# Kernel tuning notes

Hardware: AMD Instinct MI355X
Metric: run time of the kernel (lower is better)

Reference implementation:

```python
import jax, jax.numpy as jnp
import numpy as np

ALPHA = 0.2  # LeakyReLU negative slope
NEG_BIG = -9e15


def setup_inputs() -> dict:
    key = jax.random.key(0)
    k1, k2, k3, k4 = jax.random.split(key, 4)
    B, N, Fin, Fout = 16, 1024, 256, 256
    h = jax.random.normal(k1, (B, N, Fin), dtype=jnp.float32)
    adj = jax.random.randint(k2, (B, N, N), 0, 2, dtype=jnp.int32)
    # xavier_uniform with gain=1.414
    def xavier(k, shape, gain=1.414):
        fan_in, fan_out = shape[0], shape[1]
        bound = gain * np.sqrt(6.0 / (fan_in + fan_out))
        return jax.random.uniform(k, shape, jnp.float32, -bound, bound)
    W = xavier(k3, (Fin, Fout))
    a = xavier(k4, (2 * Fout, 1))
    return {"h": h, "adj": adj, "W": W, "a": a}


def reference(h, adj, W, a):
    # h: [B,N,Fin], adj: [B,N,N], W: [Fin,Fout], a: [2*Fout,1]
    Fout = W.shape[1]
    Wh = jnp.einsum('bnf,fo->bno', h, W)                      # [B,N,Fout]
    a1, a2 = a[:Fout, 0], a[Fout:, 0]                          # [Fout], [Fout]
    # e_ij = leakyrelu(Wh_i . a1 + Wh_j . a2) -- outer sum, no O(N^2*F) tensor
    f1 = Wh @ a1                                               # [B,N]
    f2 = Wh @ a2                                               # [B,N]
    e = jax.nn.leaky_relu(f1[:, :, None] + f2[:, None, :], negative_slope=ALPHA)
    attention = jnp.where(adj > 0, e, jnp.float32(NEG_BIG))    # [B,N,N]
    attention = jax.nn.softmax(attention, axis=2)
    h_prime = jnp.einsum('bij,bjo->bio', attention, Wh)        # [B,N,Fout]
    return jax.nn.elu(h_prime)
```

## Files before the change

### kernel.cpp

```cpp
#include <hip/hip_runtime.h>
#include <hip/hip_bf16.h>

#define Bsz 16
#define Nn  1024
#define Ff  256
#define ALPHA 0.2f
#define NEG_BIG -9.0e15f

typedef __attribute__((ext_vector_type(8))) short short8;
typedef __attribute__((ext_vector_type(4))) float f32x4;

__device__ __forceinline__ unsigned short f2bf(float x) {
    union { __hip_bfloat16 b; unsigned short u; } cv;
    cv.b = __float2bfloat16(x);
    return cv.u;
}

__global__ __launch_bounds__(256) void gat_prep(
    const float* __restrict__ W, const float* __restrict__ a,
    float* __restrict__ w1, float* __restrict__ w2)
{
    const int t = threadIdx.x, w = t >> 6, ln = t & 63;
    __shared__ float a1s[Ff], a2s[Ff];
    a1s[t] = a[t];
    a2s[t] = a[Ff + t];
    __syncthreads();
    const int f = blockIdx.x * 4 + w;
    float s1 = 0.f, s2 = 0.f;
    #pragma unroll
    for (int c = 0; c < 4; c++) {
        const int o = ln + 64 * c;
        const float wv = W[(size_t)f * Ff + o];
        s1 += wv * a1s[o];
        s2 += wv * a2s[o];
    }
    #pragma unroll
    for (int off = 1; off < 64; off <<= 1) {
        s1 += __shfl_xor(s1, off, 64);
        s2 += __shfl_xor(s2, off, 64);
    }
    if (ln == 0) { w1[f] = s1; w2[f] = s2; }
}

__global__ __launch_bounds__(256) void pack_f(
    const float* __restrict__ h, const float* __restrict__ W,
    const float* __restrict__ w1, const float* __restrict__ w2,
    unsigned short* __restrict__ hK, unsigned short* __restrict__ WK,
    float* __restrict__ f1, float* __restrict__ f2)
{
    __shared__ float tile[32][257];
    const int id = blockIdx.x, t = threadIdx.x, w = t >> 6, ln = t & 63;
    const bool isH = (id < 512);
    const float* src;
    unsigned short* dst;
    int grow0 = 0;
    if (isH) {
        const int b = id >> 5, kt = id & 31;
        grow0 = b * Nn + kt * 32;
        src = h + (size_t)grow0 * Ff;
        dst = hK + ((size_t)(b * 32 + kt)) * 8192;
    } else {
        const int ft = id - 512;
        src = W + (size_t)ft * 32 * Ff;
        dst = WK + (size_t)ft * 8192;
    }
    #pragma unroll
    for (int rr = 0; rr < 8; rr++) {
        const int row = rr * 4 + w;
        const int col = ln * 4;
        const float4 v = *(const float4*)&src[row * Ff + col];
        tile[row][col] = v.x; tile[row][col + 1] = v.y;
        tile[row][col + 2] = v.z; tile[row][col + 3] = v.w;
    }
    __syncthreads();

    unsigned* d32 = (unsigned*)dst;
    #pragma unroll
    for (int k = 0; k < 16; k++) {
        const int fidx = k * 256 + t;
        const int o = fidx >> 4, q = fidx & 15;
        const unsigned lo = f2bf(tile[2 * q][o]);
        const unsigned hi = f2bf(tile[2 * q + 1][o]);
        d32[fidx] = lo | (hi << 16);
    }

    if (isH) {
        float w1r[4], w2r[4];
        #pragma unroll
        for (int c = 0; c < 4; c++) {
            w1r[c] = w1[ln + 64 * c];
            w2r[c] = w2[ln + 64 * c];
        }
        #pragma unroll
        for (int rr = 0; rr < 8; rr++) {
            const int row = rr * 4 + w;
            float s1 = 0.f, s2 = 0.f;
            #pragma unroll
            for (int c = 0; c < 4; c++) {
                const float hv = tile[row][ln + 64 * c];
                s1 += hv * w1r[c];
                s2 += hv * w2r[c];
            }
            #pragma unroll
            for (int off = 1; off < 64; off <<= 1) {
                s1 += __shfl_xor(s1, off, 64);
                s2 += __shfl_xor(s2, off, 64);
            }
            if (ln == 0) { f1[grow0 + row] = s1; f2[grow0 + row] = s2; }
        }
    }
}

#define TI 16
__global__ __launch_bounds__(256, 4) void gat_attn(
    const int* __restrict__ adj,
    const float* __restrict__ f1, const float* __restrict__ f2,
    const unsigned short* __restrict__ hK, const unsigned short* __restrict__ WK,
    float* __restrict__ out)
{
    __shared__ unsigned short smem[TI * 1032];
    const int t = threadIdx.x, w = t >> 6, ln = t & 63;
    const int m = ln & 15, quad = ln >> 4;
    const int bid = blockIdx.x;
    const int b  = 2 * (bid & 7) + ((bid >> 3) & 1);
    const int i0 = (bid >> 4) * TI;

    float f2r[16];
    #pragma unroll
    for (int c = 0; c < 16; c++) f2r[c] = f2[b * Nn + ln + 64 * c];

    #pragma unroll
    for (int p = 0; p < 2; p++) {
        const int r0 = w * 4 + 2 * p, r1 = r0 + 1;
        const int gr0 = b * Nn + i0 + r0;
        const int* a0 = adj + (size_t)gr0 * Nn;
        const int* a1p = adj + (size_t)(gr0 + 1) * Nn;
        int av0[16], av1[16];
        #pragma unroll
        for (int c = 0; c < 16; c++) {
            av0[c] = a0[ln + 64 * c];
            av1[c] = a1p[ln + 64 * c];
        }
        const float fi0 = f1[gr0], fi1 = f1[gr0 + 1];
        float e0[16], e1[16];
        float mx0 = -INFINITY, mx1 = -INFINITY;
        #pragma unroll
        for (int c = 0; c < 16; c++) {
            float e = fi0 + f2r[c];
            e = (e > 0.f) ? e : ALPHA * e;
            e = (av0[c] > 0) ? e : NEG_BIG;
            e0[c] = e; mx0 = fmaxf(mx0, e);
            float g = fi1 + f2r[c];
            g = (g > 0.f) ? g : ALPHA * g;
            g = (av1[c] > 0) ? g : NEG_BIG;
            e1[c] = g; mx1 = fmaxf(mx1, g);
        }
        #pragma unroll
        for (int off = 1; off < 64; off <<= 1) {
            mx0 = fmaxf(mx0, __shfl_xor(mx0, off, 64));
            mx1 = fmaxf(mx1, __shfl_xor(mx1, off, 64));
        }
        float s0 = 0.f, s1 = 0.f;
        #pragma unroll
        for (int c = 0; c < 16; c++) {
            e0[c] = __expf(e0[c] - mx0); s0 += e0[c];
            e1[c] = __expf(e1[c] - mx1); s1 += e1[c];
        }
        #pragma unroll
        for (int off = 1; off < 64; off <<= 1) {
            s0 += __shfl_xor(s0, off, 64);
            s1 += __shfl_xor(s1, off, 64);
        }
        const float ri0 = 1.f / s0, ri1 = 1.f / s1;
        #pragma unroll
        for (int c = 0; c < 16; c++) {
            smem[r0 * 1032 + ln + 64 * c] = f2bf(e0[c] * ri0);
            smem[r1 * 1032 + ln + 64 * c] = f2bf(e1[c] * ri1);
        }
    }
    __syncthreads();

    f32x4 acc[4] = {{0.f,0.f,0.f,0.f},{0.f,0.f,0.f,0.f},{0.f,0.f,0.f,0.f},{0.f,0.f,0.f,0.f}};
    const unsigned short* hKb = hK + (size_t)b * 32 * 8192;
    for (int kt = 0; kt < 32; kt++) {
        const short8 af = *(const short8*)&smem[m * 1032 + kt * 32 + quad * 8];
        #pragma unroll
        for (int nt = 0; nt < 4; nt++) {
            const int n = w * 64 + nt * 16 + m;
            const short8 bfv = *(const short8*)&hKb[(size_t)kt * 8192 + n * 32 + quad * 8];
            acc[nt] = __builtin_amdgcn_mfma_f32_16x16x32_bf16(af, bfv, acc[nt], 0, 0, 0);
        }
    }
    __syncthreads();

    #pragma unroll
    for (int nt = 0; nt < 4; nt++)
        #pragma unroll
        for (int reg = 0; reg < 4; reg++)
            smem[(quad * 4 + reg) * 264 + w * 64 + nt * 16 + m] = f2bf(acc[nt][reg]);
    __syncthreads();

    f32x4 acc2[4] = {{0.f,0.f,0.f,0.f},{0.f,0.f,0.f,0.f},{0.f,0.f,0.f,0.f},{0.f,0.f,0.f,0.f}};
    for (int kt = 0; kt < 8; kt++) {
        const short8 af = *(const short8*)&smem[m * 264 + kt * 32 + quad * 8];
        #pragma unroll
        for (int nt = 0; nt < 4; nt++) {
            const int n = w * 64 + nt * 16 + m;
            const short8 bfv = *(const short8*)&WK[(size_t)kt * 8192 + n * 32 + quad * 8];
            acc2[nt] = __builtin_amdgcn_mfma_f32_16x16x32_bf16(af, bfv, acc2[nt], 0, 0, 0);
        }
    }
    #pragma unroll
    for (int nt = 0; nt < 4; nt++) {
        #pragma unroll
        for (int reg = 0; reg < 4; reg++) {
            const int row = quad * 4 + reg;
            const int col = w * 64 + nt * 16 + m;
            float v = acc2[nt][reg];
            v = (v > 0.f) ? v : (__expf(v) - 1.0f);
            out[((size_t)(b * Nn) + i0 + row) * Ff + col] = v;
        }
    }
}

extern "C" void kernel_launch(void* const* d_in, const int* in_sizes, int n_in,
                              void* d_out, int out_size, void* d_ws, size_t ws_size,
                              hipStream_t stream)
{
    const void* h   = d_in[0];
    const void* adj = d_in[1];
    const void* W   = d_in[2];
    const void* a   = d_in[3];
    for (int i = 0; i < n_in; i++) {
        if      (in_sizes[i] == Bsz * Nn * Ff) h   = d_in[i];
        else if (in_sizes[i] == Bsz * Nn * Nn) adj = d_in[i];
        else if (in_sizes[i] == Ff * Ff)       W   = d_in[i];
        else if (in_sizes[i] == 2 * Ff)        a   = d_in[i];
    }
    float* out = (float*)d_out;

    char*  wsb = (char*)d_ws;
    float* w1  = (float*)wsb;
    float* w2  = w1 + Ff;
    float* f1  = (float*)(wsb + 4096);
    float* f2  = f1 + Bsz * Nn;
    unsigned short* hK = (unsigned short*)(wsb + 4096 + 2 * 65536);
    unsigned short* WK = hK + (size_t)Bsz * 32 * 8192;

    gat_prep<<<64, 256, 0, stream>>>((const float*)W, (const float*)a, w1, w2);
    pack_f<<<520, 256, 0, stream>>>((const float*)h, (const float*)W, w1, w2, hK, WK, f1, f2);
    gat_attn<<<Bsz * (Nn / TI), 256, 0, stream>>>((const int*)adj, f1, f2, hK, WK, out);
}
```

Measured before the change: 159.2 us.

## Double attention row tile to 32 with 512 threads, swizzled LDS and prefetch

Doubles the attention row tile per block from 16 to 32 rows using 8 waves. Each streamed bf16 Wh K-tile is now reused by twice as many rows, which halves the total hK traffic from L2. Adjacency and f2 are read as 128-bit vectors, and the bf16 probability tile is stored in LDS with an XOR swizzle instead of padding to avoid bank conflicts. The K-loop now prefetches the next A/B fragments before issuing MFMAs. In exchange the block uses 64KB of LDS, which lowers resident blocks per CU, and the grid shrinks to 512 blocks.

```diff
diff --git a/kernel.cpp b/kernel.cpp
--- a/kernel.cpp
+++ b/kernel.cpp
@@ -9,6 +9,7 @@
 
 typedef __attribute__((ext_vector_type(8))) short short8;
 typedef __attribute__((ext_vector_type(4))) float f32x4;
+typedef __attribute__((ext_vector_type(4))) unsigned short ushort4_t;
 
 __device__ __forceinline__ unsigned short f2bf(float x) {
     union { __hip_bfloat16 b; unsigned short u; } cv;
@@ -111,49 +112,52 @@
     }
 }
 
-#define TI 16
-__global__ __launch_bounds__(256, 4) void gat_attn(
+#define TI 32
+__global__ __launch_bounds__(512, 4) void gat_attn(
     const int* __restrict__ adj,
     const float* __restrict__ f1, const float* __restrict__ f2,
     const unsigned short* __restrict__ hK, const unsigned short* __restrict__ WK,
     float* __restrict__ out)
 {
-    __shared__ unsigned short smem[TI * 1032];
+    __shared__ unsigned short pbf[TI * 1024];
     const int t = threadIdx.x, w = t >> 6, ln = t & 63;
     const int m = ln & 15, quad = ln >> 4;
     const int bid = blockIdx.x;
     const int b  = 2 * (bid & 7) + ((bid >> 3) & 1);
     const int i0 = (bid >> 4) * TI;
 
-    float f2r[16];
-    #pragma unroll
-    for (int c = 0; c < 16; c++) f2r[c] = f2[b * Nn + ln + 64 * c];
+    float4 f2r[4];
+    #pragma unroll
+    for (int c = 0; c < 4; c++)
+        f2r[c] = *(const float4*)&f2[b * Nn + 256 * c + 4 * ln];
 
     #pragma unroll
     for (int p = 0; p < 2; p++) {
         const int r0 = w * 4 + 2 * p, r1 = r0 + 1;
-        const int gr0 = b * Nn + i0 + r0;
-        const int* a0 = adj + (size_t)gr0 * Nn;
-        const int* a1p = adj + (size_t)(gr0 + 1) * Nn;
-        int av0[16], av1[16];
-        #pragma unroll
-        for (int c = 0; c < 16; c++) {
-            av0[c] = a0[ln + 64 * c];
-            av1[c] = a1p[ln + 64 * c];
-        }
-        const float fi0 = f1[gr0], fi1 = f1[gr0 + 1];
+        const int gr = b * Nn + i0 + r0;
+        const int* a0 = adj + (size_t)gr * Nn;
+        const int* a1 = a0 + Nn;
+        int4 av0[4], av1[4];
+        #pragma unroll
+        for (int c = 0; c < 4; c++) {
+            av0[c] = *(const int4*)&a0[256 * c + 4 * ln];
+            av1[c] = *(const int4*)&a1[256 * c + 4 * ln];
+        }
+        const float fi0 = f1[gr], fi1 = f1[gr + 1];
         float e0[16], e1[16];
         float mx0 = -INFINITY, mx1 = -INFINITY;
         #pragma unroll
-        for (int c = 0; c < 16; c++) {
-            float e = fi0 + f2r[c];
-            e = (e > 0.f) ? e : ALPHA * e;
-            e = (av0[c] > 0) ? e : NEG_BIG;
-            e0[c] = e; mx0 = fmaxf(mx0, e);
-            float g = fi1 + f2r[c];
-            g = (g > 0.f) ? g : ALPHA * g;
-            g = (av1[c] > 0) ? g : NEG_BIG;
-            e1[c] = g; mx1 = fmaxf(mx1, g);
+        for (int c = 0; c < 4; c++) {
+            const float4 fv = f2r[c];
+            float x;
+            x = fi0 + fv.x; x = x > 0.f ? x : ALPHA * x; x = av0[c].x > 0 ? x : NEG_BIG; e0[4*c+0] = x; mx0 = fmaxf(mx0, x);
+            x = fi0 + fv.y; x = x > 0.f ? x : ALPHA * x; x = av0[c].y > 0 ? x : NEG_BIG; e0[4*c+1] = x; mx0 = fmaxf(mx0, x);
+            x = fi0 + fv.z; x = x > 0.f ? x : ALPHA * x; x = av0[c].z > 0 ? x : NEG_BIG; e0[4*c+2] = x; mx0 = fmaxf(mx0, x);
+            x = fi0 + fv.w; x = x > 0.f ? x : ALPHA * x; x = av0[c].w > 0 ? x : NEG_BIG; e0[4*c+3] = x; mx0 = fmaxf(mx0, x);
+            x = fi1 + fv.x; x = x > 0.f ? x : ALPHA * x; x = av1[c].x > 0 ? x : NEG_BIG; e1[4*c+0] = x; mx1 = fmaxf(mx1, x);
+            x = fi1 + fv.y; x = x > 0.f ? x : ALPHA * x; x = av1[c].y > 0 ? x : NEG_BIG; e1[4*c+1] = x; mx1 = fmaxf(mx1, x);
+            x = fi1 + fv.z; x = x > 0.f ? x : ALPHA * x; x = av1[c].z > 0 ? x : NEG_BIG; e1[4*c+2] = x; mx1 = fmaxf(mx1, x);
+            x = fi1 + fv.w; x = x > 0.f ? x : ALPHA * x; x = av1[c].w > 0 ? x : NEG_BIG; e1[4*c+3] = x; mx1 = fmaxf(mx1, x);
         }
         #pragma unroll
         for (int off = 1; off < 64; off <<= 1) {
@@ -173,49 +177,70 @@
         }
         const float ri0 = 1.f / s0, ri1 = 1.f / s1;
         #pragma unroll
-        for (int c = 0; c < 16; c++) {
-            smem[r0 * 1032 + ln + 64 * c] = f2bf(e0[c] * ri0);
-            smem[r1 * 1032 + ln + 64 * c] = f2bf(e1[c] * ri1);
-        }
-    }
-    __syncthreads();
-
+        for (int c = 0; c < 4; c++) {
+            const int j = 256 * c + 4 * ln;
+            ushort4_t v0 = { f2bf(e0[4*c] * ri0), f2bf(e0[4*c+1] * ri0),
+                             f2bf(e0[4*c+2] * ri0), f2bf(e0[4*c+3] * ri0) };
+            ushort4_t v1 = { f2bf(e1[4*c] * ri1), f2bf(e1[4*c+1] * ri1),
+                             f2bf(e1[4*c+2] * ri1), f2bf(e1[4*c+3] * ri1) };
+            *(ushort4_t*)&pbf[r0 * 1024 + (j ^ ((r0 & 7) << 3))] = v0;
+            *(ushort4_t*)&pbf[r1 * 1024 + (j ^ ((r1 & 7) << 3))] = v1;
+        }
+    }
+    __syncthreads();
+
+    const int mt = w & 1, n0 = (w >> 1) << 6;
+    const unsigned short* hKb = hK + (size_t)b * 32 * 8192;
+    const int arow = (mt * 16 + m) * 1024;
+    const int asw  = (m & 7) << 3;
     f32x4 acc[4] = {{0.f,0.f,0.f,0.f},{0.f,0.f,0.f,0.f},{0.f,0.f,0.f,0.f},{0.f,0.f,0.f,0.f}};
-    const unsigned short* hKb = hK + (size_t)b * 32 * 8192;
-    for (int kt = 0; kt < 32; kt++) {
-        const short8 af = *(const short8*)&smem[m * 1032 + kt * 32 + quad * 8];
+
+    short8 afc = *(const short8*)&pbf[arow + ((quad * 8) ^ asw)];
+    short8 bc[4];
+    #pragma unroll
+    for (int nt = 0; nt < 4; nt++)
+        bc[nt] = *(const short8*)&hKb[(n0 + nt * 16 + m) * 32 + quad * 8];
+    for (int kt = 0; kt < 31; kt++) {
+        const short8 afn = *(const short8*)&pbf[arow + (((kt + 1) * 32 + quad * 8) ^ asw)];
+        short8 bn[4];
+        #pragma unroll
+        for (int nt = 0; nt < 4; nt++)
+            bn[nt] = *(const short8*)&hKb[(size_t)(kt + 1) * 8192 + (n0 + nt * 16 + m) * 32 + quad * 8];
+        #pragma unroll
+        for (int nt = 0; nt < 4; nt++)
+            acc[nt] = __builtin_amdgcn_mfma_f32_16x16x32_bf16(afc, bc[nt], acc[nt], 0, 0, 0);
+        afc = afn;
+        #pragma unroll
+        for (int nt = 0; nt < 4; nt++) bc[nt] = bn[nt];
+    }
+    #pragma unroll
+    for (int nt = 0; nt < 4; nt++)
+        acc[nt] = __builtin_amdgcn_mfma_f32_16x16x32_bf16(afc, bc[nt], acc[nt], 0, 0, 0);
+
+    __syncthreads();
+    #pragma unroll
+    for (int nt = 0; nt < 4; nt++)
+        #pragma unroll
+        for (int reg = 0; reg < 4; reg++)
+            pbf[(mt * 16 + quad * 4 + reg) * 264 + n0 + nt * 16 + m] = f2bf(acc[nt][reg]);
+    __syncthreads();
+
+    f32x4 acc2[4] = {{0.f,0.f,0.f,0.f},{0.f,0.f,0.f,0.f},{0.f,0.f,0.f,0.f},{0.f,0.f,0.f,0.f}};
+    #pragma unroll
+    for (int kt = 0; kt < 8; kt++) {
+        const short8 af = *(const short8*)&pbf[(mt * 16 + m) * 264 + kt * 32 + quad * 8];
         #pragma unroll
         for (int nt = 0; nt < 4; nt++) {
-            const int n = w * 64 + nt * 16 + m;
-            const short8 bfv = *(const short8*)&hKb[(size_t)kt * 8192 + n * 32 + quad * 8];
-            acc[nt] = __builtin_amdgcn_mfma_f32_16x16x32_bf16(af, bfv, acc[nt], 0, 0, 0);
-        }
-    }
-    __syncthreads();
-
-    #pragma unroll
-    for (int nt = 0; nt < 4; nt++)
-        #pragma unroll
-        for (int reg = 0; reg < 4; reg++)
-            smem[(quad * 4 + reg) * 264 + w * 64 + nt * 16 + m] = f2bf(acc[nt][reg]);
-    __syncthreads();
-
-    f32x4 acc2[4] = {{0.f,0.f,0.f,0.f},{0.f,0.f,0.f,0.f},{0.f,0.f,0.f,0.f},{0.f,0.f,0.f,0.f}};
-    for (int kt = 0; kt < 8; kt++) {
-        const short8 af = *(const short8*)&smem[m * 264 + kt * 32 + quad * 8];
-        #pragma unroll
-        for (int nt = 0; nt < 4; nt++) {
-            const int n = w * 64 + nt * 16 + m;
-            const short8 bfv = *(const short8*)&WK[(size_t)kt * 8192 + n * 32 + quad * 8];
-            acc2[nt] = __builtin_amdgcn_mfma_f32_16x16x32_bf16(af, bfv, acc2[nt], 0, 0, 0);
+            const short8 bv = *(const short8*)&WK[(size_t)kt * 8192 + (n0 + nt * 16 + m) * 32 + quad * 8];
+            acc2[nt] = __builtin_amdgcn_mfma_f32_16x16x32_bf16(af, bv, acc2[nt], 0, 0, 0);
         }
     }
     #pragma unroll
     for (int nt = 0; nt < 4; nt++) {
         #pragma unroll
         for (int reg = 0; reg < 4; reg++) {
-            const int row = quad * 4 + reg;
-            const int col = w * 64 + nt * 16 + m;
+            const int row = mt * 16 + quad * 4 + reg;
+            const int col = n0 + nt * 16 + m;
             float v = acc2[nt][reg];
             v = (v > 0.f) ? v : (__expf(v) - 1.0f);
             out[((size_t)(b * Nn) + i0 + row) * Ff + col] = v;
@@ -249,5 +274,5 @@
 
     gat_prep<<<64, 256, 0, stream>>>((const float*)W, (const float*)a, w1, w2);
     pack_f<<<520, 256, 0, stream>>>((const float*)h, (const float*)W, w1, w2, hK, WK, f1, f2);
-    gat_attn<<<Bsz * (Nn / TI), 256, 0, stream>>>((const int*)adj, f1, f2, hK, WK, out);
-}
+    gat_attn<<<Bsz * (Nn / TI), 512, 0, stream>>>((const int*)adj, f1, f2, hK, WK, out);
+}
```

Result: no change. 158.1 us (-0.7%).
